# Kernel tuning notes

Hardware: AMD Instinct MI355X
Metric: run time of the kernel (lower is better)

Reference implementation:

```python
import jax, jax.numpy as jnp
import numpy as np

N = 100000
E = 6400000
H = 64  # hidden_nf


def setup_inputs() -> dict:
    key = jax.random.key(0)
    ks = jax.random.split(key, 12)
    x = jax.random.normal(ks[0], (N, 3), dtype=jnp.float32)
    vel = jax.random.normal(ks[1], (N, 3), dtype=jnp.float32)
    vel_norm = jax.random.uniform(ks[2], (N, 1), dtype=jnp.float32)
    edge_index = jax.random.randint(ks[3], (2, E), 0, N, dtype=jnp.int32)
    # coord_mlp_vel: Linear(1,H) -> LeakyReLU(0.2) -> Linear(H,1)
    W1 = jax.random.normal(ks[4], (H, 1), dtype=jnp.float32) * (1.0 / np.sqrt(1))
    b1 = jnp.zeros((H,), dtype=jnp.float32)
    W2 = jax.random.normal(ks[5], (1, H), dtype=jnp.float32) * (1.0 / np.sqrt(H))
    b2 = jnp.zeros((1,), dtype=jnp.float32)
    # phi: Linear(1,H) -> LeakyReLU(0.2) -> Linear(H,1,bias=False, xavier gain=0.001) -> Tanh
    Wp1 = jax.random.normal(ks[6], (H, 1), dtype=jnp.float32) * (1.0 / np.sqrt(1))
    bp1 = jnp.zeros((H,), dtype=jnp.float32)
    Wp2 = jax.random.normal(ks[7], (1, H), dtype=jnp.float32) * 0.001
    return {"x": x, "vel_norm": vel_norm, "vel": vel, "edge_index": edge_index,
            "W1": W1, "b1": b1, "W2": W2, "b2": b2,
            "Wp1": Wp1, "bp1": bp1, "Wp2": Wp2}


def reference(x, vel_norm, vel, edge_index, W1, b1, W2, b2, Wp1, bp1, Wp2):
    row, col = edge_index[0], edge_index[1]
    # edge_model: gather endpoint positions, radial distance -> tiny MLP -> scaled diff
    x_diff = x[row] - x[col]                                   # [E, 3]
    radial = jnp.sqrt(jnp.sum(x_diff * x_diff, axis=1, keepdims=True))  # [E, 1]
    h = jax.nn.leaky_relu(radial @ Wp1.T + bp1, 0.2)           # [E, H]
    e_out = jnp.tanh(h @ Wp2.T)                                # [E, 1]
    m_ij = x_diff * e_out                                      # [E, 3]
    # node_model: unsorted_segment_mean over row
    agg_sum = jax.ops.segment_sum(m_ij, row, num_segments=x.shape[0])           # [N, 3]
    cnt = jax.ops.segment_sum(jnp.ones((m_ij.shape[0], 1), m_ij.dtype), row,
                              num_segments=x.shape[0])                           # [N, 1]
    x_out = x + agg_sum / jnp.maximum(cnt, 1.0)
    # velocity term: x + vel * coord_mlp_vel(vel_norm)
    hv = jax.nn.leaky_relu(vel_norm @ W1.T + b1, 0.2)          # [N, H]
    scale = hv @ W2.T + b2                                     # [N, 1]
    return x_out + vel * scale
```

## Files before the change

### kernel.cpp

```cpp
#include <hip/hip_runtime.h>
#include <hip/hip_fp16.h>
#include <math.h>

#define LEAKY 0.2f
#define HDIM 64
#define EPB 4096
#define TPB1 256
#define PERT (EPB / TPB1)
#define RANGE 1024
#define RSH 10
#define KMAX 128
#define NSUB 4
#define NSLICE 16
#define FS2 262144.0f
#define INVFS2 (1.0f / 262144.0f)
#define FBIAS 4194304


__device__ __forceinline__ float fast_tanh(float v) {
    float e = __builtin_amdgcn_exp2f(v * 2.88539008178f);
    return 1.0f - 2.0f * __builtin_amdgcn_rcpf(e + 1.0f);
}

__device__ __noinline__ float edge_eo_slow(float rad,
                                           const float* sW1, const float* sb1,
                                           const float* sW2) {
    float a = 0.f;
    #pragma unroll 1
    for (int k = 0; k < HDIM; k++) {
        float h = fmaf(rad, sW1[k], sb1[k]);
        h = (h > 0.f) ? h : LEAKY * h;
        a = fmaf(sW2[k], h, a);
    }
    return fast_tanh(a);
}

__global__ void repack_h_kernel(const float* __restrict__ x, uint2* __restrict__ xh, int N,
                                const float* __restrict__ Wp1, const float* __restrict__ bp1,
                                const float* __restrict__ Wp2, float* __restrict__ consts,
                                uint4* __restrict__ acc4, unsigned* __restrict__ cursor, int K) {
    int i = blockIdx.x * blockDim.x + threadIdx.x;
    if (i < N) {
        unsigned hx = __half_as_ushort(__float2half(x[3*i]));
        unsigned hy = __half_as_ushort(__float2half(x[3*i+1]));
        unsigned hz = __half_as_ushort(__float2half(x[3*i+2]));
        xh[i] = make_uint2((hy << 16) | hx, hz);
        acc4[i] = make_uint4(0u, 0u, 0u, 0u);
    }
    if (blockIdx.x == 0) {
        if (threadIdx.x < 64) {
            int k = threadIdx.x;
            float w1 = Wp1[k];
            float slope = (w1 >= 0.f) ? 1.f : LEAKY;
            float c = Wp2[k] * w1 * slope;
            float bnz = (bp1[k] != 0.f) ? 1.f : 0.f;
            #pragma unroll
            for (int off = 32; off > 0; off >>= 1) {
                c += __shfl_down(c, off, 64);
                bnz += __shfl_down(bnz, off, 64);
            }
            if (k == 0) { consts[0] = c; consts[1] = bnz; }
        }
        for (int k = threadIdx.x; k < NSUB * K; k += 256) cursor[k] = 0u;
    }
}

__device__ __noinline__ void overflow_edge(unsigned rec, unsigned b_, const uint2* __restrict__ xh,
                              float C, bool slow,
                              const float* __restrict__ Wp1, const float* __restrict__ bp1,
                              const float* __restrict__ Wp2, unsigned* __restrict__ acc4) {
    unsigned lid = rec >> 17, col = rec & 0x1FFFFu;
    unsigned row = b_ * RANGE + lid;
    uint2 ga = xh[row], gb = xh[col];
    float ax = __half2float(__ushort_as_half((unsigned short)(ga.x & 0xFFFF)));
    float ay = __half2float(__ushort_as_half((unsigned short)(ga.x >> 16)));
    float az = __half2float(__ushort_as_half((unsigned short)(ga.y & 0xFFFF)));
    float bx = __half2float(__ushort_as_half((unsigned short)(gb.x & 0xFFFF)));
    float by = __half2float(__ushort_as_half((unsigned short)(gb.x >> 16)));
    float bz = __half2float(__ushort_as_half((unsigned short)(gb.y & 0xFFFF)));
    float dx = ax - bx, dy = ay - by, dz = az - bz;
    float rad = sqrtf(dx*dx + dy*dy + dz*dz);
    float eo;
    if (!slow) {
        eo = fast_tanh(C * rad);
    } else {
        float a = 0.f;
        for (int k = 0; k < HDIM; k++) {
            float h = fmaf(rad, Wp1[k], bp1[k]);
            h = (h > 0.f) ? h : LEAKY * h;
            a = fmaf(Wp2[k], h, a);
        }
        eo = fast_tanh(a);
    }
    atomicAdd(&acc4[4*row + 0], (unsigned)__float2int_rn(dx * eo * FS2));
    atomicAdd(&acc4[4*row + 1], (unsigned)__float2int_rn(dy * eo * FS2));
    atomicAdd(&acc4[4*row + 2], (unsigned)__float2int_rn(dz * eo * FS2));
    atomicAdd(&acc4[4*row + 3], 1u);
}

__global__ __launch_bounds__(TPB1) void sort4_kernel(
        const int* __restrict__ ei,
        const uint2* __restrict__ xh,
        const float* __restrict__ Wp1, const float* __restrict__ bp1,
        const float* __restrict__ Wp2, const float* __restrict__ consts,
        unsigned* __restrict__ cursor, unsigned* __restrict__ acc4,
        unsigned* __restrict__ recs, int E, int K, unsigned csub) {
    __shared__ unsigned stage[EPB];
    __shared__ unsigned char bucket_of[EPB];
    __shared__ unsigned hist[KMAX];
    __shared__ unsigned scanv[KMAX + 1];
    __shared__ unsigned cur[KMAX];
    __shared__ unsigned gstart[KMAX];
    const float C = consts[0];
    const bool slow = (consts[1] != 0.f);
    const unsigned sub = (unsigned)blockIdx.x & (NSUB - 1);
    for (int k = threadIdx.x; k < K; k += TPB1) hist[k] = 0;
    __syncthreads();

    const size_t base = (size_t)blockIdx.x * EPB;
    const unsigned t = threadIdx.x;
    unsigned rc[PERT];
    unsigned bk[PERT];
    if (base + EPB <= (size_t)E && (E & 3) == 0) {
        const int4* pr = (const int4*)(ei + base);
        const int4* pc = (const int4*)(ei + (size_t)E + base);
        #pragma unroll
        for (int q = 0; q < PERT / 4; q++) {
            int4 rv = pr[t + q * TPB1];
            int4 cv = pc[t + q * TPB1];
            rc[4*q+0] = (((unsigned)rv.x & (RANGE-1)) << 17) | (unsigned)cv.x;
            rc[4*q+1] = (((unsigned)rv.y & (RANGE-1)) << 17) | (unsigned)cv.y;
            rc[4*q+2] = (((unsigned)rv.z & (RANGE-1)) << 17) | (unsigned)cv.z;
            rc[4*q+3] = (((unsigned)rv.w & (RANGE-1)) << 17) | (unsigned)cv.w;
            bk[4*q+0] = (unsigned)rv.x >> RSH;
            bk[4*q+1] = (unsigned)rv.y >> RSH;
            bk[4*q+2] = (unsigned)rv.z >> RSH;
            bk[4*q+3] = (unsigned)rv.w >> RSH;
        }
        #pragma unroll
        for (int i = 0; i < PERT; i++) atomicAdd(&hist[bk[i]], 1u);
    } else {
        #pragma unroll
        for (int i = 0; i < PERT; i++) {
            size_t e = base + (size_t)i * TPB1 + t;
            bk[i] = 0xFFFFFFFFu;
            if (e < (size_t)E) {
                unsigned r = (unsigned)ei[e];
                unsigned c = (unsigned)ei[(size_t)E + e];
                rc[i] = ((r & (RANGE-1)) << 17) | c;
                bk[i] = r >> RSH;
                atomicAdd(&hist[bk[i]], 1u);
            }
        }
    }
    __syncthreads();
    unsigned res = 0;
    if (t < (unsigned)K) {
        unsigned myc = hist[t];
        if (myc) res = atomicAdd(&cursor[t * NSUB + sub], myc);
    }
    if (t >= 192) {
        int l = t - 192;
        unsigned origA = (l < K) ? hist[l] : 0u;
        unsigned origB = (l + 64 < K) ? hist[l + 64] : 0u;
        unsigned a = origA, b = origB;
        #pragma unroll
        for (int off = 1; off < 64; off <<= 1) {
            unsigned va = __shfl_up(a, off, 64);
            unsigned vb = __shfl_up(b, off, 64);
            if (l >= off) { a += va; b += vb; }
        }
        unsigned totA = __shfl(a, 63, 64);
        unsigned grand = totA + __shfl(b, 63, 64);
        unsigned exA = a - origA;
        unsigned exB = totA + b - origB;
        scanv[l] = exA;  cur[l] = exA;
        scanv[l + 64] = exB;  cur[l + 64] = exB;
        if (l == 63) scanv[K] = grand;
    }
    __syncthreads();
    #pragma unroll
    for (int i = 0; i < PERT; i++) {
        if (bk[i] != 0xFFFFFFFFu) {
            unsigned slot = atomicAdd(&cur[bk[i]], 1u);
            stage[slot] = rc[i];
            bucket_of[slot] = (unsigned char)bk[i];
        }
    }
    if (t < (unsigned)K) gstart[t] = res;
    __syncthreads();
    unsigned total = scanv[K];
    for (unsigned j = t; j < total; j += TPB1) {
        unsigned b_ = bucket_of[j];
        unsigned off = gstart[b_] + (j - scanv[b_]);
        if (off < csub) recs[(size_t)(b_ * NSUB + sub) * csub + off] = stage[j];
        else            overflow_edge(stage[j], b_, xh, C, slow, Wp1, bp1, Wp2, acc4);
    }
}

__global__ __launch_bounds__(256, 4) void reduce7_kernel(
        const unsigned* __restrict__ recs, const unsigned* __restrict__ cursor,
        const uint2* __restrict__ xh,
        const float* __restrict__ Wp1, const float* __restrict__ bp1,
        const float* __restrict__ Wp2, const float* __restrict__ consts,
        uint4* __restrict__ slices, int N, int K, unsigned csub) {
    __shared__ unsigned long long accA[RANGE];
    __shared__ unsigned long long accB[RANGE];
    __shared__ uint2 sxh[RANGE];
    __shared__ float sW1[HDIM], sb1[HDIM], sW2[HDIM];
    const int b = blockIdx.x / NSLICE;
    const int s = blockIdx.x % NSLICE;
    const int r = s & (NSUB - 1);
    const int p = s >> 2;
    const float C = consts[0];
    const bool slow = (consts[1] != 0.f);
    const int nbase = b * RANGE;
    if (slow) {
        for (int k = threadIdx.x; k < HDIM; k += 256) {
            sW1[k] = Wp1[k]; sb1[k] = bp1[k]; sW2[k] = Wp2[k];
        }
    }
    for (int i = threadIdx.x; i < RANGE; i += 256) {
        accA[i] = 0ull; accB[i] = 0ull;
        int src = nbase + i;
        sxh[i] = xh[(src < N) ? src : 0];
    }
    __syncthreads();
    unsigned cnt = cursor[b * NSUB + r];
    if (cnt > csub) cnt = csub;
    unsigned quads = (cnt + 3) >> 2;
    unsigned perq = (quads + 3) >> 2;
    unsigned q0 = (unsigned)p * perq;
    unsigned q1 = q0 + perq; if (q1 > quads) q1 = quads;
    const uint4* rb4 = (const uint4*)(recs + (size_t)(b * NSUB + r) * csub);

    #define PROC_REC(rec, idx)                                                     \
        if ((idx) < cnt) {                                                         \
            unsigned lid_ = (rec) >> 17, col_ = (rec) & 0x1FFFFu;                  \
            uint2 ga = sxh[lid_];                                                  \
            uint2 gb = xh[col_];                                                   \
            float ax = __half2float(__ushort_as_half((unsigned short)(ga.x & 0xFFFF))); \
            float ay = __half2float(__ushort_as_half((unsigned short)(ga.x >> 16)));    \
            float az = __half2float(__ushort_as_half((unsigned short)(ga.y & 0xFFFF))); \
            float bx = __half2float(__ushort_as_half((unsigned short)(gb.x & 0xFFFF))); \
            float by = __half2float(__ushort_as_half((unsigned short)(gb.x >> 16)));    \
            float bz = __half2float(__ushort_as_half((unsigned short)(gb.y & 0xFFFF))); \
            float dx = ax - bx, dy = ay - by, dz = az - bz;                        \
            float rad = sqrtf(dx*dx + dy*dy + dz*dz);                              \
            float eo = slow ? edge_eo_slow(rad, sW1, sb1, sW2)                     \
                            : fast_tanh(C * rad);                                  \
            unsigned ix = (unsigned)(__float2int_rn(dx * eo * FS2) + FBIAS);       \
            unsigned iy = (unsigned)(__float2int_rn(dy * eo * FS2) + FBIAS);       \
            unsigned iz = (unsigned)(__float2int_rn(dz * eo * FS2) + FBIAS);       \
            atomicAdd(&accA[lid_], ((unsigned long long)ix << 32) | (unsigned long long)iy); \
            atomicAdd(&accB[lid_], ((unsigned long long)iz << 32) | 1ull);         \
        }

    unsigned q = q0 + threadIdx.x;
    while (q + 256 < q1) {
        uint4 v0 = rb4[q];
        uint4 v1 = rb4[q + 256];
        unsigned i0 = 4 * q, i1 = 4 * (q + 256);
        PROC_REC(v0.x, i0); PROC_REC(v0.y, i0 + 1);
        PROC_REC(v0.z, i0 + 2); PROC_REC(v0.w, i0 + 3);
        PROC_REC(v1.x, i1); PROC_REC(v1.y, i1 + 1);
        PROC_REC(v1.z, i1 + 2); PROC_REC(v1.w, i1 + 3);
        q += 512;
    }
    while (q < q1) {
        uint4 v = rb4[q];
        unsigned i0 = 4 * q;
        PROC_REC(v.x, i0); PROC_REC(v.y, i0 + 1);
        PROC_REC(v.z, i0 + 2); PROC_REC(v.w, i0 + 3);
        q += 256;
    }
    #undef PROC_REC
    __syncthreads();
    for (int i = threadIdx.x; i < RANGE; i += 256) {
        int node = nbase + i;
        if (node < N) {
            unsigned long long A = accA[i], B = accB[i];
            slices[(size_t)s * N + node] =
                make_uint4((unsigned)(A >> 32), (unsigned)A,
                           (unsigned)(B >> 32), (unsigned)B);
        }
    }
}

__global__ void node_merge_kernel(const float* __restrict__ x,
                                  const float* __restrict__ vel_norm,
                                  const float* __restrict__ vel,
                                  const float* __restrict__ W1, const float* __restrict__ b1,
                                  const float* __restrict__ W2, const float* __restrict__ b2,
                                  const uint4* __restrict__ slices,
                                  const uint4* __restrict__ acc4,
                                  float* __restrict__ out, int N) {
    __shared__ float sW1[HDIM], sb1[HDIM], sW2[HDIM];
    for (int k = threadIdx.x; k < HDIM; k += blockDim.x) {
        sW1[k] = W1[k]; sb1[k] = b1[k]; sW2[k] = W2[k];
    }
    __syncthreads();
    int i = blockIdx.x * blockDim.x + threadIdx.x;
    if (i >= N) return;
    unsigned long long sxb = 0, syb = 0, szb = 0;
    unsigned sc = 0;
    #pragma unroll
    for (int s = 0; s < NSLICE; s++) {
        uint4 v = slices[(size_t)s * N + i];
        sxb += v.x; syb += v.y; szb += v.z; sc += v.w;
    }
    uint4 a4 = acc4[i];
    long long fx = (long long)sxb - (long long)sc * (long long)FBIAS + (long long)(int)a4.x;
    long long fy = (long long)syb - (long long)sc * (long long)FBIAS + (long long)(int)a4.y;
    long long fz = (long long)szb - (long long)sc * (long long)FBIAS + (long long)(int)a4.z;
    float cntf = (float)(sc + a4.w);
    float sx = (float)fx * INVFS2;
    float sy = (float)fy * INVFS2;
    float sz = (float)fz * INVFS2;
    float vn = vel_norm[i];
    float a = b2[0];
    #pragma unroll
    for (int k = 0; k < HDIM; k++) {
        float h = fmaf(vn, sW1[k], sb1[k]);
        h = (h > 0.f) ? h : LEAKY * h;
        a = fmaf(sW2[k], h, a);
    }
    float inv = 1.0f / fmaxf(cntf, 1.0f);
    out[3*i]     = x[3*i]     + sx * inv + vel[3*i]     * a;
    out[3*i + 1] = x[3*i + 1] + sy * inv + vel[3*i + 1] * a;
    out[3*i + 2] = x[3*i + 2] + sz * inv + vel[3*i + 2] * a;
}

__global__ void precompute_kernel(const float* __restrict__ Wp1,
                                  const float* __restrict__ bp1,
                                  const float* __restrict__ Wp2,
                                  float* __restrict__ consts) {
    int k = threadIdx.x;
    float w1 = Wp1[k];
    float slope = (w1 >= 0.f) ? 1.f : LEAKY;
    float c = Wp2[k] * w1 * slope;
    float bnz = (bp1[k] != 0.f) ? 1.f : 0.f;
    #pragma unroll
    for (int off = 32; off > 0; off >>= 1) {
        c += __shfl_down(c, off, 64);
        bnz += __shfl_down(bnz, off, 64);
    }
    if (k == 0) { consts[0] = c; consts[1] = bnz; }
}

__global__ void edge_atomic_kernel(const float* __restrict__ x, const int* __restrict__ ei,
                                   const float* __restrict__ Wp1, const float* __restrict__ bp1,
                                   const float* __restrict__ Wp2, const float* __restrict__ consts,
                                   float* __restrict__ acc, int E) {
    __shared__ float sW1[HDIM], sb1[HDIM], sW2[HDIM];
    const float C = consts[0];
    const bool slow = (consts[1] != 0.f);
    if (slow) {
        for (int k = threadIdx.x; k < HDIM; k += blockDim.x) {
            sW1[k] = Wp1[k]; sb1[k] = bp1[k]; sW2[k] = Wp2[k];
        }
        __syncthreads();
    }
    int e = blockIdx.x * blockDim.x + threadIdx.x;
    if (e >= E) return;
    int r = ei[e];
    int c = ei[E + e];
    float dx = x[3*r] - x[3*c];
    float dy = x[3*r+1] - x[3*c+1];
    float dz = x[3*r+2] - x[3*c+2];
    float rad = sqrtf(dx*dx + dy*dy + dz*dz);
    float eo;
    if (!slow) {
        eo = fast_tanh(C * rad);
    } else {
        float a = 0.f;
        for (int k = 0; k < HDIM; k++) {
            float h = fmaf(rad, sW1[k], sb1[k]);
            h = (h > 0.f) ? h : LEAKY * h;
            a = fmaf(sW2[k], h, a);
        }
        eo = fast_tanh(a);
    }
    float* basep = acc + ((size_t)r << 2);
    atomicAdd(basep + 0, dx * eo);
    atomicAdd(basep + 1, dy * eo);
    atomicAdd(basep + 2, dz * eo);
    atomicAdd(basep + 3, 1.f);
}

__global__ void node_kernel(const float* __restrict__ x, const float* __restrict__ vel_norm,
                            const float* __restrict__ vel,
                            const float* __restrict__ W1, const float* __restrict__ b1,
                            const float* __restrict__ W2, const float* __restrict__ b2,
                            const float4* __restrict__ slices,
                            float* __restrict__ out, int N, int S) {
    __shared__ float sW1[HDIM], sb1[HDIM], sW2[HDIM];
    for (int k = threadIdx.x; k < HDIM; k += blockDim.x) {
        sW1[k] = W1[k]; sb1[k] = b1[k]; sW2[k] = W2[k];
    }
    __syncthreads();
    int i = blockIdx.x * blockDim.x + threadIdx.x;
    if (i >= N) return;
    float sx = 0.f, sy = 0.f, sz = 0.f, sc = 0.f;
    for (int s = 0; s < S; s++) {
        float4 v = slices[(size_t)s * N + i];
        sx += v.x; sy += v.y; sz += v.z; sc += v.w;
    }
    float vn = vel_norm[i];
    float a = b2[0];
    #pragma unroll
    for (int k = 0; k < HDIM; k++) {
        float h = fmaf(vn, sW1[k], sb1[k]);
        h = (h > 0.f) ? h : LEAKY * h;
        a = fmaf(sW2[k], h, a);
    }
    float inv = 1.0f / fmaxf(sc, 1.0f);
    out[3*i]     = x[3*i]     + sx * inv + vel[3*i]     * a;
    out[3*i + 1] = x[3*i + 1] + sy * inv + vel[3*i + 1] * a;
    out[3*i + 2] = x[3*i + 2] + sz * inv + vel[3*i + 2] * a;
}

extern "C" void kernel_launch(void* const* d_in, const int* in_sizes, int n_in,
                              void* d_out, int out_size, void* d_ws, size_t ws_size,
                              hipStream_t stream) {
    const float* x        = (const float*)d_in[0];
    const float* vel_norm = (const float*)d_in[1];
    const float* vel      = (const float*)d_in[2];
    const int*   ei       = (const int*)  d_in[3];
    const float* W1       = (const float*)d_in[4];
    const float* b1       = (const float*)d_in[5];
    const float* W2       = (const float*)d_in[6];
    const float* b2       = (const float*)d_in[7];
    const float* Wp1      = (const float*)d_in[8];
    const float* bp1      = (const float*)d_in[9];
    const float* Wp2      = (const float*)d_in[10];

    const int N = in_sizes[0] / 3;
    const int E = in_sizes[3] / 2;
    const int K = (N + RANGE - 1) / RANGE;
    const int nblk = (E + EPB - 1) / EPB;

    unsigned csub = (unsigned)(E / (K * NSUB)) + 1024u;
    csub = (csub + 63u) & ~63u;

    size_t rec_bytes = (size_t)K * NSUB * csub * sizeof(unsigned);
    size_t sp_slices = (rec_bytes + 15) & ~(size_t)15;
    size_t sp_xh     = sp_slices + (size_t)NSLICE * N * sizeof(uint4);
    size_t sp_acc    = (sp_xh + (size_t)N * sizeof(uint2) + 15) & ~(size_t)15;
    size_t sp_cur    = sp_acc + (size_t)N * sizeof(uint4);
    size_t sp_const  = (sp_cur + (size_t)NSUB * KMAX * sizeof(unsigned) + 15) & ~(size_t)15;
    size_t need      = sp_const + 32;

    if (K <= KMAX && ws_size >= need) {
        unsigned* recs   = (unsigned*)d_ws;
        uint4*    slices = (uint4*)   ((char*)d_ws + sp_slices);
        uint2*    xh     = (uint2*)   ((char*)d_ws + sp_xh);
        unsigned* acc4   = (unsigned*)((char*)d_ws + sp_acc);
        unsigned* cursor = (unsigned*)((char*)d_ws + sp_cur);
        float*    consts = (float*)   ((char*)d_ws + sp_const);

        repack_h_kernel<<<(N + 255) / 256, 256, 0, stream>>>(
            x, xh, N, Wp1, bp1, Wp2, consts, (uint4*)acc4, cursor, K);
        sort4_kernel<<<nblk, TPB1, 0, stream>>>(
            ei, xh, Wp1, bp1, Wp2, consts, cursor, acc4, recs, E, K, csub);
        reduce7_kernel<<<K * NSLICE, 256, 0, stream>>>(
            recs, cursor, xh, Wp1, bp1, Wp2, consts, slices, N, K, csub);
        node_merge_kernel<<<(N + 255) / 256, 256, 0, stream>>>(
            x, vel_norm, vel, W1, b1, W2, b2, slices, (const uint4*)acc4,
            (float*)d_out, N);
    } else {
        float* acc    = (float*)d_ws;
        float* consts = (float*)((char*)d_ws + (size_t)N * sizeof(float4));
        hipMemsetAsync(d_ws, 0, (size_t)N * sizeof(float4) + 32, stream);
        precompute_kernel<<<1, 64, 0, stream>>>(Wp1, bp1, Wp2, consts);
        edge_atomic_kernel<<<(E + 255) / 256, 256, 0, stream>>>(x, ei, Wp1, bp1, Wp2,
                                                                consts, acc, E);
        node_kernel<<<(N + 255) / 256, 256, 0, stream>>>(x, vel_norm, vel, W1, b1, W2, b2,
                                                         (const float4*)acc, (float*)d_out, N, 1);
    }
}
```

Baseline: 183.5 us.

## Use histogram atomic ranks for scatter, wave-per-bucket writeout, more reduce partitions

The sort kernel now keeps the return value of the histogram atomic as each edge's rank inside its bucket. That lets it place records without a second atomic cursor pass or a bucket_of array, and each wave then copies whole buckets to global memory in contiguous runs. The reduce kernel splits each sub-bucket across 6 partitions instead of 4. It also drops the shared-memory staging of source-node coordinates and reads them from global memory (L2/cache) instead. The intent is less LDS atomic traffic, more coalesced writes and more reduce parallelism, at the cost of more global reads per edge and more slice buffers for the merge kernel to combine.

After: 197.3 us. +7.5%, slower.

```diff
diff --git a/kernel.cpp b/kernel.cpp
--- a/kernel.cpp
+++ b/kernel.cpp
@@ -11,7 +11,8 @@
 #define RSH 10
 #define KMAX 128
 #define NSUB 4
-#define NSLICE 16
+#define NPART 6
+#define NSLICE (NSUB * NPART)
 #define FS2 262144.0f
 #define INVFS2 (1.0f / 262144.0f)
 #define FBIAS 4194304
@@ -98,7 +99,7 @@
     atomicAdd(&acc4[4*row + 3], 1u);
 }
 
-__global__ __launch_bounds__(TPB1) void sort4_kernel(
+__global__ __launch_bounds__(TPB1) void sort5_kernel(
         const int* __restrict__ ei,
         const uint2* __restrict__ xh,
         const float* __restrict__ Wp1, const float* __restrict__ bp1,
@@ -106,10 +107,8 @@
         unsigned* __restrict__ cursor, unsigned* __restrict__ acc4,
         unsigned* __restrict__ recs, int E, int K, unsigned csub) {
     __shared__ unsigned stage[EPB];
-    __shared__ unsigned char bucket_of[EPB];
     __shared__ unsigned hist[KMAX];
     __shared__ unsigned scanv[KMAX + 1];
-    __shared__ unsigned cur[KMAX];
     __shared__ unsigned gstart[KMAX];
     const float C = consts[0];
     const bool slow = (consts[1] != 0.f);
@@ -120,7 +119,7 @@
     const size_t base = (size_t)blockIdx.x * EPB;
     const unsigned t = threadIdx.x;
     unsigned rc[PERT];
-    unsigned bk[PERT];
+    unsigned meta[PERT];
     if (base + EPB <= (size_t)E && (E & 3) == 0) {
         const int4* pr = (const int4*)(ei + base);
         const int4* pc = (const int4*)(ei + (size_t)E + base);
@@ -132,24 +131,26 @@
             rc[4*q+1] = (((unsigned)rv.y & (RANGE-1)) << 17) | (unsigned)cv.y;
             rc[4*q+2] = (((unsigned)rv.z & (RANGE-1)) << 17) | (unsigned)cv.z;
             rc[4*q+3] = (((unsigned)rv.w & (RANGE-1)) << 17) | (unsigned)cv.w;
-            bk[4*q+0] = (unsigned)rv.x >> RSH;
-            bk[4*q+1] = (unsigned)rv.y >> RSH;
-            bk[4*q+2] = (unsigned)rv.z >> RSH;
-            bk[4*q+3] = (unsigned)rv.w >> RSH;
-        }
-        #pragma unroll
-        for (int i = 0; i < PERT; i++) atomicAdd(&hist[bk[i]], 1u);
+            unsigned b0 = (unsigned)rv.x >> RSH;
+            unsigned b1 = (unsigned)rv.y >> RSH;
+            unsigned b2 = (unsigned)rv.z >> RSH;
+            unsigned b3 = (unsigned)rv.w >> RSH;
+            meta[4*q+0] = (b0 << 12) | atomicAdd(&hist[b0], 1u);
+            meta[4*q+1] = (b1 << 12) | atomicAdd(&hist[b1], 1u);
+            meta[4*q+2] = (b2 << 12) | atomicAdd(&hist[b2], 1u);
+            meta[4*q+3] = (b3 << 12) | atomicAdd(&hist[b3], 1u);
+        }
     } else {
         #pragma unroll
         for (int i = 0; i < PERT; i++) {
             size_t e = base + (size_t)i * TPB1 + t;
-            bk[i] = 0xFFFFFFFFu;
+            meta[i] = 0xFFFFFFFFu;
             if (e < (size_t)E) {
                 unsigned r = (unsigned)ei[e];
                 unsigned c = (unsigned)ei[(size_t)E + e];
                 rc[i] = ((r & (RANGE-1)) << 17) | c;
-                bk[i] = r >> RSH;
-                atomicAdd(&hist[bk[i]], 1u);
+                unsigned b_ = r >> RSH;
+                meta[i] = (b_ << 12) | atomicAdd(&hist[b_], 1u);
             }
         }
     }
@@ -172,33 +173,37 @@
         }
         unsigned totA = __shfl(a, 63, 64);
         unsigned grand = totA + __shfl(b, 63, 64);
-        unsigned exA = a - origA;
-        unsigned exB = totA + b - origB;
-        scanv[l] = exA;  cur[l] = exA;
-        scanv[l + 64] = exB;  cur[l + 64] = exB;
+        scanv[l] = a - origA;
+        scanv[l + 64] = totA + b - origB;
         if (l == 63) scanv[K] = grand;
     }
     __syncthreads();
     #pragma unroll
     for (int i = 0; i < PERT; i++) {
-        if (bk[i] != 0xFFFFFFFFu) {
-            unsigned slot = atomicAdd(&cur[bk[i]], 1u);
-            stage[slot] = rc[i];
-            bucket_of[slot] = (unsigned char)bk[i];
+        if (meta[i] != 0xFFFFFFFFu) {
+            unsigned bk_ = meta[i] >> 12;
+            stage[scanv[bk_] + (meta[i] & 0xFFFu)] = rc[i];
         }
     }
     if (t < (unsigned)K) gstart[t] = res;
     __syncthreads();
-    unsigned total = scanv[K];
-    for (unsigned j = t; j < total; j += TPB1) {
-        unsigned b_ = bucket_of[j];
-        unsigned off = gstart[b_] + (j - scanv[b_]);
-        if (off < csub) recs[(size_t)(b_ * NSUB + sub) * csub + off] = stage[j];
-        else            overflow_edge(stage[j], b_, xh, C, slow, Wp1, bp1, Wp2, acc4);
-    }
-}
-
-__global__ __launch_bounds__(256, 4) void reduce7_kernel(
+    {
+        const int wv = t >> 6, ln = (int)(t & 63u);
+        for (int b_ = wv; b_ < K; b_ += 4) {
+            unsigned lo = scanv[b_], hi = scanv[b_ + 1];
+            unsigned gb = gstart[b_];
+            unsigned* dst = recs + (size_t)(b_ * NSUB + sub) * csub;
+            for (unsigned j = lo + ln; j < hi; j += 64) {
+                unsigned off = gb + (j - lo);
+                if (off < csub) dst[off] = stage[j];
+                else            overflow_edge(stage[j], (unsigned)b_, xh, C, slow,
+                                              Wp1, bp1, Wp2, acc4);
+            }
+        }
+    }
+}
+
+__global__ __launch_bounds__(256, 4) void reduce8_kernel(
         const unsigned* __restrict__ recs, const unsigned* __restrict__ cursor,
         const uint2* __restrict__ xh,
         const float* __restrict__ Wp1, const float* __restrict__ bp1,
@@ -206,7 +211,6 @@
         uint4* __restrict__ slices, int N, int K, unsigned csub) {
     __shared__ unsigned long long accA[RANGE];
     __shared__ unsigned long long accB[RANGE];
-    __shared__ uint2 sxh[RANGE];
     __shared__ float sW1[HDIM], sb1[HDIM], sW2[HDIM];
     const int b = blockIdx.x / NSLICE;
     const int s = blockIdx.x % NSLICE;
@@ -220,16 +224,12 @@
             sW1[k] = Wp1[k]; sb1[k] = bp1[k]; sW2[k] = Wp2[k];
         }
     }
-    for (int i = threadIdx.x; i < RANGE; i += 256) {
-        accA[i] = 0ull; accB[i] = 0ull;
-        int src = nbase + i;
-        sxh[i] = xh[(src < N) ? src : 0];
-    }
+    for (int i = threadIdx.x; i < RANGE; i += 256) { accA[i] = 0ull; accB[i] = 0ull; }
     __syncthreads();
     unsigned cnt = cursor[b * NSUB + r];
     if (cnt > csub) cnt = csub;
     unsigned quads = (cnt + 3) >> 2;
-    unsigned perq = (quads + 3) >> 2;
+    unsigned perq = (quads + NPART - 1) / NPART;
     unsigned q0 = (unsigned)p * perq;
     unsigned q1 = q0 + perq; if (q1 > quads) q1 = quads;
     const uint4* rb4 = (const uint4*)(recs + (size_t)(b * NSUB + r) * csub);
@@ -237,7 +237,7 @@
     #define PROC_REC(rec, idx)                                                     \
         if ((idx) < cnt) {                                                         \
             unsigned lid_ = (rec) >> 17, col_ = (rec) & 0x1FFFFu;                  \
-            uint2 ga = sxh[lid_];                                                  \
+            uint2 ga = xh[nbase + (int)lid_];                                      \
             uint2 gb = xh[col_];                                                   \
             float ax = __half2float(__ushort_as_half((unsigned short)(ga.x & 0xFFFF))); \
             float ay = __half2float(__ushort_as_half((unsigned short)(ga.x >> 16)));    \
@@ -461,9 +461,9 @@
 
         repack_h_kernel<<<(N + 255) / 256, 256, 0, stream>>>(
             x, xh, N, Wp1, bp1, Wp2, consts, (uint4*)acc4, cursor, K);
-        sort4_kernel<<<nblk, TPB1, 0, stream>>>(
+        sort5_kernel<<<nblk, TPB1, 0, stream>>>(
             ei, xh, Wp1, bp1, Wp2, consts, cursor, acc4, recs, E, K, csub);
-        reduce7_kernel<<<K * NSLICE, 256, 0, stream>>>(
+        reduce8_kernel<<<K * NSLICE, 256, 0, stream>>>(
             recs, cursor, xh, Wp1, bp1, Wp2, consts, slices, N, K, csub);
         node_merge_kernel<<<(N + 255) / 256, 256, 0, stream>>>(
             x, vel_norm, vel, W1, b1, W2, b2, slices, (const uint4*)acc4,
```
